# Kernel optimization log

Hardware: AMD Instinct MI355X
Metric: run time of the kernel (lower is better)

Reference implementation:

```python
import jax, jax.numpy as jnp
import numpy as np

G = 4      # groups (conv groups == offset groups)
KS = 3     # kernel size
DIL = 1    # dilation
PAD = 1    # padding = dilation
EPS = 1e-5 # InstanceNorm eps


def setup_inputs() -> dict:
    key = jax.random.key(0)
    k1, k2, k3, k4, k5 = jax.random.split(key, 5)
    B, C, D, H, W = 4, 64, 8, 64, 64
    Cout = 64
    Cg = C // G
    x = jax.random.normal(k1, (B, C, D, H, W), jnp.float32)
    # small offset-conv weights so predicted offsets stay within a few pixels
    w_off = jax.random.normal(k2, (2 * KS * KS * G, Cg, KS, KS), jnp.float32) * 0.01
    b_off = jax.random.normal(k3, (2 * KS * KS * G,), jnp.float32) * 0.01
    w_dc = jax.random.normal(k4, (Cout, Cg, KS, KS), jnp.float32) * (1.0 / np.sqrt(Cg * KS * KS))
    b_dc = jax.random.normal(k5, (Cout,), jnp.float32) * 0.01
    return {"x": x, "w_off": w_off, "b_off": b_off, "w_dc": w_dc, "b_dc": b_dc}


def reference(x, w_off, b_off, w_dc, b_dc):
    B, C, D, H, W = x.shape
    N = B * D
    K = KS * KS
    Cg = C // G
    # torch .view(B*D, C, H, W) is a row-major reshape of the flat buffer
    x2 = x.reshape(N, C, H, W)

    # grouped 3x3 offset conv, same padding
    off = jax.lax.conv_general_dilated(
        x2, w_off, (1, 1), [(PAD, PAD), (PAD, PAD)],
        rhs_dilation=(DIL, DIL), feature_group_count=G,
        dimension_numbers=("NCHW", "OIHW", "NCHW"),
    ) + b_off[None, :, None, None]
    off = off.reshape(N, G, K, 2, H, W)        # (y, x) offset per group/kernel-pt
    dy, dx = off[:, :, :, 0], off[:, :, :, 1]  # [N,G,K,H,W]

    # base sampling grid per kernel point
    ki, kj = jnp.meshgrid(jnp.arange(KS), jnp.arange(KS), indexing="ij")
    ki = ki.reshape(K); kj = kj.reshape(K)
    base_y = (jnp.arange(H)[None, :] - PAD + ki[:, None] * DIL).astype(jnp.float32)  # [K,H]
    base_x = (jnp.arange(W)[None, :] - PAD + kj[:, None] * DIL).astype(jnp.float32)  # [K,W]
    py = base_y[None, None, :, :, None] + dy   # [N,G,K,H,W]
    px = base_x[None, None, :, None, :] + dx

    y0 = jnp.floor(py); x0 = jnp.floor(px)
    ly = py - y0; lx = px - x0
    y0i = y0.astype(jnp.int32); x0i = x0.astype(jnp.int32)

    xg = x2.reshape(N, G, Cg, H * W)
    gather = jax.vmap(jax.vmap(lambda xf, idx: xf[:, idx]))  # over N, G

    def corner(yi, xi, w):
        valid = (yi >= 0) & (yi < H) & (xi >= 0) & (xi < W)   # zero-pad OOB
        idx = jnp.clip(yi, 0, H - 1) * W + jnp.clip(xi, 0, W - 1)
        v = gather(xg, idx.reshape(N, G, -1)).reshape(N, G, Cg, K, H, W)
        return v * (w * valid)[:, :, None]                    # broadcast over Cg

    val = (corner(y0i,     x0i,     (1 - ly) * (1 - lx))
         + corner(y0i,     x0i + 1, (1 - ly) * lx)
         + corner(y0i + 1, x0i,     ly * (1 - lx))
         + corner(y0i + 1, x0i + 1, ly * lx))                 # [N,G,Cg,K,H,W]

    wg = w_dc.reshape(G, -1, Cg, K)                           # [G,Coutg,Cg,K]
    out = jnp.einsum("gock,ngckhw->ngohw", wg, val).reshape(N, -1, H, W)
    out = out + b_dc[None, :, None, None]

    # InstanceNorm2d (affine=False, biased var) + exact GELU
    m = out.mean((-2, -1), keepdims=True)
    v = out.var((-2, -1), keepdims=True)
    out = jax.nn.gelu((out - m) * jax.lax.rsqrt(v + EPS), approximate=False)

    Cout = out.shape[1]
    return out.reshape(B, D, Cout, H, W).transpose(0, 2, 1, 3, 4)  # [B,Cout,D,H,W]
```

## Files before the change

### kernel.cpp

```cpp
#include <hip/hip_runtime.h>
#include <hip/hip_fp16.h>
#include <math.h>

#define HW 4096
#define NN 32
#define W68 68

typedef __attribute__((ext_vector_type(8))) _Float16 f16x8;
typedef __attribute__((ext_vector_type(2))) _Float16 h2;
typedef __attribute__((ext_vector_type(4))) float f32x4;

__device__ inline unsigned short hbits(float a) {
    _Float16 h = (_Float16)a;
    unsigned short u;
    __builtin_memcpy(&u, &h, 2);
    return u;
}
__device__ inline unsigned hpack(float a, float b) {
    auto p = __builtin_amdgcn_cvt_pkrtz(a, b);
    unsigned u;
    __builtin_memcpy(&u, &p, 4);
    return u;
}

__device__ inline int xsw(int x, int c8) {
    return ((x << 5) | (c8 << 4)) ^ (((x >> 2) & 1) << 4);
}

__global__ __launch_bounds__(256) void wperm_build(const float* __restrict__ w_off,
                                                   const float* __restrict__ w_dc,
                                                   unsigned short* __restrict__ wperm)
{
    int idx = blockIdx.x * 256 + threadIdx.x;
    int g = idx / 7680;
    int r3 = idx - g * 7680;
    int which = r3 / 2560;
    int r = r3 - which * 2560;
    int j = r & 7;
    int rest = r >> 3;
    int nn_ = rest & 15; rest >>= 4;
    int q_ = rest & 3, kp_ = rest >> 2;
    int k = q_ * 8 + j;
    int c = k & 15, tt = kp_ * 2 + (k >> 4);
    float v = 0.f;
    if (tt < 9) {
        if (which == 0)      v = w_dc[(g * 16 + nn_) * 144 + c * 9 + tt];
        else if (which == 1) v = w_off[(g * 18 + nn_) * 144 + c * 9 + tt];
        else if (nn_ < 2)    v = w_off[(g * 18 + 16 + nn_) * 144 + c * 9 + tt];
    }
    wperm[idx] = hbits(v);
}

__global__ __launch_bounds__(256, 4) void fused_conv(const float* __restrict__ x,
                                                     const unsigned short* __restrict__ wperm,
                                                     const float* __restrict__ b_off,
                                                     const float* __restrict__ b_dc,
                                                     unsigned short* __restrict__ outpre)
{
    __shared__ __attribute__((aligned(16))) unsigned short xwin[10240];
    __shared__ __attribute__((aligned(8)))  unsigned short off_lds[256 * 20];

    int bhw = blockIdx.x;
    int bx = (bhw & 7) * 256 + (bhw >> 3);
    int n = bx >> 6, g = (bx >> 4) & 3, chunk = bx & 15;
    int t = threadIdx.x;
    int lane = t & 63, wv = t >> 6;
    int nn = lane & 15, q = lane >> 4;
    int t2 = q >> 1, chh = q & 1;
    int R0 = chunk * 4;

    const unsigned short* wpg = wperm + g * 7680;
    const float* xgbase = x + (size_t)(n * 64 + g * 16) * HW;

    {
        int col = lane;
        #pragma unroll
        for (int rr = 0; rr < 2; rr++) {
            int r = wv * 2 + rr;
            int h = R0 + r - 2;
            uint4 lo = {0, 0, 0, 0}, hi = {0, 0, 0, 0};
            if ((unsigned)h < 64u) {
                const float* xp = xgbase + h * 64 + col;
                float v[16];
                #pragma unroll
                for (int c = 0; c < 16; c++) v[c] = xp[(size_t)c * HW];
                lo.x = hpack(v[0], v[1]);  lo.y = hpack(v[2], v[3]);
                lo.z = hpack(v[4], v[5]);  lo.w = hpack(v[6], v[7]);
                hi.x = hpack(v[8], v[9]);  hi.y = hpack(v[10], v[11]);
                hi.z = hpack(v[12], v[13]); hi.w = hpack(v[14], v[15]);
            }
            *(uint4*)((char*)xwin + r * 2176 + xsw(col + 2, 0)) = lo;
            *(uint4*)((char*)xwin + r * 2176 + xsw(col + 2, 1)) = hi;
        }
        {
            int h = R0 + 6;
            unsigned a = 0, b = 0;
            if (h < 64) {
                const float* xp = xgbase + (size_t)(wv * 4) * HW + h * 64 + col;
                a = hpack(xp[0], xp[HW]);
                b = hpack(xp[2 * HW], xp[3 * HW]);
            }
            char* p = (char*)xwin + 8 * 2176 + xsw(col + 2, wv >> 1) + (wv & 1) * 8;
            *(unsigned*)p = a;
            *(unsigned*)(p + 4) = b;
        }
        if (t < 72) {
            int r = t >> 3, rem = t & 7;
            int xc = rem >> 1, c8 = rem & 1;
            int xx = xc < 2 ? xc : xc + 64;
            uint4 z = {0, 0, 0, 0};
            *(uint4*)((char*)xwin + r * 2176 + xsw(xx, c8)) = z;
        }
    }

    int pls[4]; float fy[4], fx[4]; int rws[4], xbs[4];
    #pragma unroll
    for (int s = 0; s < 4; s++) {
        int pl = (wv * 4 + s) * 16 + nn;
        int pos = chunk * 256 + pl;
        int h = pos >> 6, w = pos & 63;
        pls[s] = pl;
        fy[s] = (float)(h - 1);
        fx[s] = (float)(w - 1);
        rws[s] = ((wv * 4 + s) >> 2) + 1;
        xbs[s] = ((wv * 4 + s) & 3) * 16 + nn + 1;
    }

    __syncthreads();

    {
        f16x8 pb0[5], pb1[5];
        #pragma unroll
        for (int kp = 0; kp < 5; kp++) {
            int fo = ((kp * 4 + q) * 16 + nn) * 8;
            pb0[kp] = *(const f16x8*)(wpg + 2560 + fo);
            pb1[kp] = *(const f16x8*)(wpg + 5120 + fo);
        }

        f32x4 acc0[4], acc1[4];
        float bv0 = b_off[g * 18 + nn];
        float bv1 = (nn < 2) ? b_off[g * 18 + 16 + nn] : 0.f;
        #pragma unroll
        for (int s = 0; s < 4; s++)
            #pragma unroll
            for (int r = 0; r < 4; r++) { acc0[s][r] = bv0; acc1[s][r] = bv1; }

        uint4 xv[2][4];
        auto stage1 = [&](int kp) {
            int ki = t2 ? (2 * kp + 1) / 3 : (2 * kp) / 3;
            int kj = t2 ? (2 * kp + 1) % 3 : (2 * kp) % 3;
            int sl = kp & 1;
            #pragma unroll
            for (int s = 0; s < 4; s++) {
                int adr = (rws[s] + ki) * 2176 + xsw(xbs[s] + kj, chh);
                xv[sl][s] = *(const uint4*)((const char*)xwin + adr);
            }
        };
        stage1(0);
        #pragma unroll
        for (int kp = 0; kp < 5; kp++) {
            if (kp < 4) stage1(kp + 1);
            __builtin_amdgcn_sched_barrier(0);
            int sl = kp & 1;
            #pragma unroll
            for (int s = 0; s < 4; s++) {
                f16x8 af = *(f16x8*)&xv[sl][s];
                acc0[s] = __builtin_amdgcn_mfma_f32_16x16x32_f16(af, pb0[kp], acc0[s], 0, 0, 0);
                acc1[s] = __builtin_amdgcn_mfma_f32_16x16x32_f16(af, pb1[kp], acc1[s], 0, 0, 0);
            }
        }

        #pragma unroll
        for (int s = 0; s < 4; s++) {
            int pl = (wv * 4 + s) * 16 + q * 4;
            #pragma unroll
            for (int r = 0; r < 4; r++) {
                off_lds[(pl + r) * 20 + nn] = hbits(acc0[s][r]);
                if (nn < 2)
                    off_lds[(pl + r) * 20 + 16 + nn] = hbits(acc1[s][r]);
            }
        }
        off_lds[t * 20 + 18] = 0;
        off_lds[t * 20 + 19] = 0;
    }

    f16x8 bwr[5];
    #pragma unroll
    for (int kp = 0; kp < 5; kp++)
        bwr[kp] = *(const f16x8*)(wpg + ((kp * 4 + q) * 16 + nn) * 8);

    __syncthreads();

    f32x4 acc[4];
    float bv = b_dc[g * 16 + nn];
    #pragma unroll
    for (int s = 0; s < 4; s++)
        #pragma unroll
        for (int r = 0; r < 4; r++) acc[s][r] = bv;

    uint4 RA[3], RB[3], RC[3], RD[3];
    h2 rwh[3][4];
    int rinw[3], rgy[3], rgx[3];

    auto gather_x = [&](int R, int C) -> uint4 {
        uint4 out = {0, 0, 0, 0};
        int h = R - 2, w = C - 2;
        if ((unsigned)h < 64u && (unsigned)w < 64u) {
            const float* xp = xgbase + (size_t)(chh * 8) * HW + h * 64 + w;
            unsigned* o = (unsigned*)&out;
            #pragma unroll
            for (int k = 0; k < 4; k++)
                o[k] = hpack(xp[(size_t)(2 * k) * HW], xp[(size_t)(2 * k + 1) * HW]);
        }
        return out;
    };

    auto stage = [&](int u) {
        int kp = u >> 2, s = u & 3, sl = u % 3;
        int ki = t2 ? (2 * kp + 1) / 3 : (2 * kp) / 3;
        int kj = t2 ? (2 * kp + 1) % 3 : (2 * kp) % 3;
        unsigned uo = *(const unsigned*)&off_lds[pls[s] * 20 + 4 * kp + 2 * t2];
        h2 oo;
        __builtin_memcpy(&oo, &uo, 4);
        float py = fy[s] + (float)ki + (float)oo[0];
        float px = fx[s] + (float)kj + (float)oo[1];
        float y0f = fminf(fmaxf(floorf(py), -2.f), 64.f);
        float x0f = fminf(fmaxf(floorf(px), -2.f), 64.f);
        float ly = py - y0f, lx = px - x0f;
        float my = 1.f - ly, mx = 1.f - lx;
        rwh[sl][0] = h2{(_Float16)(my * mx), (_Float16)(my * mx)};
        rwh[sl][1] = h2{(_Float16)(my * lx), (_Float16)(my * lx)};
        rwh[sl][2] = h2{(_Float16)(ly * mx), (_Float16)(ly * mx)};
        rwh[sl][3] = h2{(_Float16)(ly * lx), (_Float16)(ly * lx)};
        int y0 = (int)y0f, x0 = (int)x0f;
        int lr = y0 + 2 - R0;
        int inw = ((unsigned)lr <= 7u);
        int lrc = inw ? lr : 0;
        int xx = x0 + 2;
        int a0 = lrc * 2176 + xsw(xx, chh);
        int a1 = lrc * 2176 + xsw(xx + 1, chh);
        RA[sl] = *(const uint4*)((const char*)xwin + a0);
        RB[sl] = *(const uint4*)((const char*)xwin + a1);
        RC[sl] = *(const uint4*)((const char*)xwin + a0 + 2176);
        RD[sl] = *(const uint4*)((const char*)xwin + a1 + 2176);
        rinw[sl] = inw;
        rgy[sl] = y0 + 2;
        rgx[sl] = xx;
    };
    auto consume = [&](int u) {
        int kp = u >> 2, s = u & 3, sl = u % 3;
        if (!__all(rinw[sl])) {
            if (!rinw[sl]) {
                int R = rgy[sl], C = rgx[sl];
                RA[sl] = gather_x(R, C);
                RB[sl] = gather_x(R, C + 1);
                RC[sl] = gather_x(R + 1, C);
                RD[sl] = gather_x(R + 1, C + 1);
            }
        }
        const h2* A2 = (const h2*)&RA[sl];
        const h2* B2 = (const h2*)&RB[sl];
        const h2* C2 = (const h2*)&RC[sl];
        const h2* D2 = (const h2*)&RD[sl];
        h2 w0 = rwh[sl][0], w1 = rwh[sl][1], w2 = rwh[sl][2], w3 = rwh[sl][3];
        uint4 afu;
        unsigned* au = (unsigned*)&afu;
        #pragma unroll
        for (int j = 0; j < 4; j++) {
            h2 v = w0 * A2[j] + w1 * B2[j] + w2 * C2[j] + w3 * D2[j];
            __builtin_memcpy(&au[j], &v, 4);
        }
        f16x8 af = *(f16x8*)&afu;
        acc[s] = __builtin_amdgcn_mfma_f32_16x16x32_f16(af, bwr[kp], acc[s], 0, 0, 0);
    };

    stage(0);
    stage(1);
    #pragma unroll
    for (int u = 0; u < 20; u++) {
        if (u < 18) stage(u + 2);
        __builtin_amdgcn_sched_barrier(0);
        consume(u);
    }

    unsigned short* op = outpre + (size_t)(n * 64 + g * 16) * HW;
    #pragma unroll
    for (int s = 0; s < 4; s++) {
        int pbase = chunk * 256 + (wv * 4 + s) * 16 + q * 4;
        uint2 pk;
        pk.x = hpack(acc[s][0], acc[s][1]);
        pk.y = hpack(acc[s][2], acc[s][3]);
        *(uint2*)(op + (size_t)nn * HW + pbase) = pk;
    }
}

__global__ __launch_bounds__(256) void norm_gelu(const unsigned short* __restrict__ outpre,
                                                 float* __restrict__ out)
{
    __shared__ float red[8];
    int bhw = blockIdx.x;
    int bx = (bhw & 7) * 256 + (bhw >> 3);
    int n  = bx >> 6;
    int co = bx & 63;
    int t  = threadIdx.x;

    const uint2* base = (const uint2*)(outpre + (size_t)(n * 64 + co) * HW);
    float4 v[4];
    float s = 0.f, sq = 0.f;
    #pragma unroll
    for (int r = 0; r < 4; r++) {
        uint2 u2 = base[t + r * 256];
        h2 p0, p1;
        __builtin_memcpy(&p0, &u2.x, 4);
        __builtin_memcpy(&p1, &u2.y, 4);
        v[r].x = (float)p0[0]; v[r].y = (float)p0[1];
        v[r].z = (float)p1[0]; v[r].w = (float)p1[1];
        s  += v[r].x + v[r].y + v[r].z + v[r].w;
        sq  = fmaf(v[r].x, v[r].x, sq);
        sq  = fmaf(v[r].y, v[r].y, sq);
        sq  = fmaf(v[r].z, v[r].z, sq);
        sq  = fmaf(v[r].w, v[r].w, sq);
    }
    #pragma unroll
    for (int o2 = 32; o2 > 0; o2 >>= 1) {
        s  += __shfl_down(s,  o2, 64);
        sq += __shfl_down(sq, o2, 64);
    }
    int wid = t >> 6, lane = t & 63;
    if (lane == 0) { red[wid] = s; red[4 + wid] = sq; }
    __syncthreads();
    float S  = red[0] + red[1] + red[2] + red[3];
    float SQ = red[4] + red[5] + red[6] + red[7];
    float mean = S * (1.f / 4096.f);
    float var  = SQ * (1.f / 4096.f) - mean * mean;
    float rstd = rsqrtf(var + 1e-5f);

    int b = n >> 3, d = n & 7;
    float4* outp = (float4*)(out + ((size_t)(b * 64 + co) * 8 + d) * HW);
    #pragma unroll
    for (int r = 0; r < 4; r++) {
        float xs[4] = {v[r].x, v[r].y, v[r].z, v[r].w};
        float4 res;
        float* rp = (float*)&res;
        #pragma unroll
        for (int qq = 0; qq < 4; qq++) {
            float xn = (xs[qq] - mean) * rstd;
            float u = xn * (1.5957691f + 0.0713548162f * xn * xn);
            float e = __expf(-u);
            rp[qq] = xn * __frcp_rn(1.f + e);
        }
        outp[t + r * 256] = res;
    }
}

extern "C" void kernel_launch(void* const* d_in, const int* in_sizes, int n_in,
                              void* d_out, int out_size, void* d_ws, size_t ws_size,
                              hipStream_t stream) {
    const float* x     = (const float*)d_in[0];
    const float* w_off = (const float*)d_in[1];
    const float* w_dc  = (const float*)d_in[3];
    float* out = (float*)d_out;

    unsigned short* wperm = (unsigned short*)d_ws;
    unsigned short* outpre = (unsigned short*)((char*)d_ws + 61440);

    wperm_build<<<120, 256, 0, stream>>>(w_off, w_dc, wperm);
    fused_conv <<<2048, 256, 0, stream>>>(x, wperm,
                                          (const float*)d_in[2],
                                          (const float*)d_in[4], outpre);
    norm_gelu  <<<2048, 256, 0, stream>>>(outpre, out);
}
```

Measured before the change: 125.7 us.

## Pad LDS row stride, shorten gather pipeline, and stage output stores through LDS

Changes the LDS row stride of the input window from 2176 to 2192 bytes, likely to spread bank accesses, and shrinks the xwin buffer. It cuts the deformable-gather software pipeline from three register slots to two, which lowers register pressure but hides less latency. The epilogue now writes the fp16 accumulators into LDS (reusing off_lds) and then emits coalesced 16-byte global stores instead of scattered 8-byte stores. The cost is two extra barriers at the end of the kernel.

```diff
diff --git a/kernel.cpp b/kernel.cpp
--- a/kernel.cpp
+++ b/kernel.cpp
@@ -5,6 +5,7 @@
 #define HW 4096
 #define NN 32
 #define W68 68
+#define RSTR 2192
 
 typedef __attribute__((ext_vector_type(8))) _Float16 f16x8;
 typedef __attribute__((ext_vector_type(2))) _Float16 h2;
@@ -57,8 +58,8 @@
                                                      const float* __restrict__ b_dc,
                                                      unsigned short* __restrict__ outpre)
 {
-    __shared__ __attribute__((aligned(16))) unsigned short xwin[10240];
-    __shared__ __attribute__((aligned(8)))  unsigned short off_lds[256 * 20];
+    __shared__ __attribute__((aligned(16))) unsigned short xwin[9864];
+    __shared__ __attribute__((aligned(16))) unsigned short off_lds[256 * 20];
 
     int bhw = blockIdx.x;
     int bx = (bhw & 7) * 256 + (bhw >> 3);
@@ -89,8 +90,8 @@
                 hi.x = hpack(v[8], v[9]);  hi.y = hpack(v[10], v[11]);
                 hi.z = hpack(v[12], v[13]); hi.w = hpack(v[14], v[15]);
             }
-            *(uint4*)((char*)xwin + r * 2176 + xsw(col + 2, 0)) = lo;
-            *(uint4*)((char*)xwin + r * 2176 + xsw(col + 2, 1)) = hi;
+            *(uint4*)((char*)xwin + r * RSTR + xsw(col + 2, 0)) = lo;
+            *(uint4*)((char*)xwin + r * RSTR + xsw(col + 2, 1)) = hi;
         }
         {
             int h = R0 + 6;
@@ -100,7 +101,7 @@
                 a = hpack(xp[0], xp[HW]);
                 b = hpack(xp[2 * HW], xp[3 * HW]);
             }
-            char* p = (char*)xwin + 8 * 2176 + xsw(col + 2, wv >> 1) + (wv & 1) * 8;
+            char* p = (char*)xwin + 8 * RSTR + xsw(col + 2, wv >> 1) + (wv & 1) * 8;
             *(unsigned*)p = a;
             *(unsigned*)(p + 4) = b;
         }
@@ -109,7 +110,7 @@
             int xc = rem >> 1, c8 = rem & 1;
             int xx = xc < 2 ? xc : xc + 64;
             uint4 z = {0, 0, 0, 0};
-            *(uint4*)((char*)xwin + r * 2176 + xsw(xx, c8)) = z;
+            *(uint4*)((char*)xwin + r * RSTR + xsw(xx, c8)) = z;
         }
     }
 
@@ -152,7 +153,7 @@
             int sl = kp & 1;
             #pragma unroll
             for (int s = 0; s < 4; s++) {
-                int adr = (rws[s] + ki) * 2176 + xsw(xbs[s] + kj, chh);
+                int adr = (rws[s] + ki) * RSTR + xsw(xbs[s] + kj, chh);
                 xv[sl][s] = *(const uint4*)((const char*)xwin + adr);
             }
         };
@@ -198,9 +199,9 @@
         #pragma unroll
         for (int r = 0; r < 4; r++) acc[s][r] = bv;
 
-    uint4 RA[3], RB[3], RC[3], RD[3];
-    h2 rwh[3][4];
-    int rinw[3], rgy[3], rgx[3];
+    uint4 RA[2], RB[2], RC[2], RD[2];
+    h2 rwh[2][4];
+    int rinw[2], rgy[2], rgx[2];
 
     auto gather_x = [&](int R, int C) -> uint4 {
         uint4 out = {0, 0, 0, 0};
@@ -216,7 +217,7 @@
     };
 
     auto stage = [&](int u) {
-        int kp = u >> 2, s = u & 3, sl = u % 3;
+        int kp = u >> 2, s = u & 3, sl = u & 1;
         int ki = t2 ? (2 * kp + 1) / 3 : (2 * kp) / 3;
         int kj = t2 ? (2 * kp + 1) % 3 : (2 * kp) % 3;
         unsigned uo = *(const unsigned*)&off_lds[pls[s] * 20 + 4 * kp + 2 * t2];
@@ -237,18 +238,18 @@
         int inw = ((unsigned)lr <= 7u);
         int lrc = inw ? lr : 0;
         int xx = x0 + 2;
-        int a0 = lrc * 2176 + xsw(xx, chh);
-        int a1 = lrc * 2176 + xsw(xx + 1, chh);
+        int a0 = lrc * RSTR + xsw(xx, chh);
+        int a1 = lrc * RSTR + xsw(xx + 1, chh);
         RA[sl] = *(const uint4*)((const char*)xwin + a0);
         RB[sl] = *(const uint4*)((const char*)xwin + a1);
-        RC[sl] = *(const uint4*)((const char*)xwin + a0 + 2176);
-        RD[sl] = *(const uint4*)((const char*)xwin + a1 + 2176);
+        RC[sl] = *(const uint4*)((const char*)xwin + a0 + RSTR);
+        RD[sl] = *(const uint4*)((const char*)xwin + a1 + RSTR);
         rinw[sl] = inw;
         rgy[sl] = y0 + 2;
         rgx[sl] = xx;
     };
     auto consume = [&](int u) {
-        int kp = u >> 2, s = u & 3, sl = u % 3;
+        int kp = u >> 2, s = u & 3, sl = u & 1;
         if (!__all(rinw[sl])) {
             if (!rinw[sl]) {
                 int R = rgy[sl], C = rgx[sl];
@@ -275,22 +276,30 @@
     };
 
     stage(0);
-    stage(1);
     #pragma unroll
     for (int u = 0; u < 20; u++) {
-        if (u < 18) stage(u + 2);
+        if (u < 19) stage(u + 1);
         __builtin_amdgcn_sched_barrier(0);
         consume(u);
     }
 
-    unsigned short* op = outpre + (size_t)(n * 64 + g * 16) * HW;
+    __syncthreads();
     #pragma unroll
     for (int s = 0; s < 4; s++) {
-        int pbase = chunk * 256 + (wv * 4 + s) * 16 + q * 4;
+        int colb = (wv * 4 + s) * 16 + q * 4;
         uint2 pk;
         pk.x = hpack(acc[s][0], acc[s][1]);
         pk.y = hpack(acc[s][2], acc[s][3]);
-        *(uint2*)(op + (size_t)nn * HW + pbase) = pk;
+        *(uint2*)(off_lds + nn * 264 + colb) = pk;
+    }
+    __syncthreads();
+    unsigned short* opb = outpre + (size_t)(n * 64 + g * 16) * HW + chunk * 256;
+    #pragma unroll
+    for (int p = 0; p < 2; p++) {
+        int idx = p * 256 + t;
+        int ch = idx >> 5, slot = idx & 31;
+        uint4 vv = *(const uint4*)(off_lds + ch * 264 + slot * 8);
+        *(uint4*)(opb + (size_t)ch * HW + slot * 8) = vv;
     }
 }
 
```

Result: faster. 122.2 us (-2.8%).
